# Kernel tuning notes

Hardware: AMD Instinct MI355X
Metric: run time of the kernel (lower is better)

The kernel has to match this reference:

```python
import jax, jax.numpy as jnp
import numpy as np

NUM_BLOCKS_TOTAL = 24  # num_layers(3) * num_blocks(8)
DIL_CYCLE = 8          # dilation = 2 ** (i % 8)


def setup_inputs() -> dict:
    key = jax.random.key(0)
    ks = jax.random.split(key, 12)
    B, C, S, Tq = 256, 32, 32, 256  # batch, residual_ch, skip_ch, queue length
    w = lambda k, sh: jax.random.normal(k, sh, jnp.float32) * 0.1
    return {
        "queues": jax.random.normal(ks[0], (NUM_BLOCKS_TOTAL, B, C, Tq), jnp.float32),
        "x": jax.random.normal(ks[1], (B, 1, 1), jnp.float32),
        "num": jax.random.normal(ks[2], (B, 8, 1), jnp.float32),
        "cat": jax.random.randint(ks[3], (B, 1, 1), 0, 1000),
        "emb_table": w(ks[4], (1000, 16)),
        "W_in": w(ks[5], (C, 25)), "b_in": jnp.zeros((C,), jnp.float32),
        "W_conv": w(ks[6], (NUM_BLOCKS_TOTAL, 2 * C, C, 2)),
        "b_conv": jnp.zeros((NUM_BLOCKS_TOTAL, 2 * C), jnp.float32),
        "W_res": w(ks[7], (NUM_BLOCKS_TOTAL, C, C)),
        "b_res": jnp.zeros((NUM_BLOCKS_TOTAL, C), jnp.float32),
        "W_skip": w(ks[8], (NUM_BLOCKS_TOTAL, S, C)),
        "b_skip": jnp.zeros((NUM_BLOCKS_TOTAL, S), jnp.float32),
        "W_o1": w(ks[9], (128, NUM_BLOCKS_TOTAL * S)), "b_o1": jnp.zeros((128,), jnp.float32),
        "W_o2": w(ks[10], (1, 128)), "b_o2": jnp.zeros((1,), jnp.float32),
    }


def reference(queues, x, num, cat, emb_table, W_in, b_in, W_conv, b_conv,
              W_res, b_res, W_skip, b_skip, W_o1, b_o1, W_o2, b_o2):
    # --- input assembly: concat(x, num, embeds(cat)) along channels, 1 timestep ---
    emb = emb_table[cat[:, 0, 0]][:, :, None]            # [B,16,1]
    inp = jnp.concatenate([x, num, emb], axis=1)          # [B,25,1]
    # pointwise input_conv (kernel_size=1)
    cur = jnp.einsum('oc,bct->bot', W_in, inp) + b_in[None, :, None]  # [B,C,1]

    new_queues = []
    skips = []
    for i in range(NUM_BLOCKS_TOTAL):
        d = 2 ** (i % DIL_CYCLE)
        q = jnp.concatenate([queues[i], cur], axis=2)     # grow queue: [B,C,Tq+1]
        new_queues.append(q)
        # fast_forward: kernel-2 dilated causal conv on last and (last - d) taps
        tap0 = q[:, :, -1 - d]                            # [B,C]
        tap1 = q[:, :, -1]                                # [B,C]
        z = tap0 @ W_conv[i, :, :, 0].T + tap1 @ W_conv[i, :, :, 1].T + b_conv[i]  # [B,2C]
        fz, gz = jnp.split(z, 2, axis=1)
        gated = jnp.tanh(fz) * jax.nn.sigmoid(gz)          # [B,C]
        skips.append(gated @ W_skip[i].T + b_skip[i])      # [B,S]
        cur = (gated @ W_res[i].T + b_res[i] + tap1)[:, :, None]  # residual -> next queue

    sk = jax.nn.relu(jnp.concatenate(skips, axis=1))       # [B, 24*S]
    sk = jax.nn.relu(sk @ W_o1.T + b_o1)                   # [B,128]
    out = (sk @ W_o2.T + b_o2)[:, :, None]                 # [B,1,1]
    return out, jnp.stack(new_queues, axis=0)
```

## Files before the change

### kernel.cpp

```cpp
#include <hip/hip_runtime.h>

#define NBLK 24
#define BATCH 256
#define CCH 32
#define TQ 256
#define TQO 257
#define NCOMP 32
#define BPG 8
#define NCOPY 3072
#define ROWS (NBLK*BATCH*CCH)

typedef float f4a4  __attribute__((ext_vector_type(4), aligned(4)));
typedef float f4a16 __attribute__((ext_vector_type(4)));

__global__ __launch_bounds__(256) void w2w_kernel(
    const float* __restrict__ qin,
    const float* __restrict__ x,
    const float* __restrict__ num,
    const int*   __restrict__ cat,
    const float* __restrict__ emb,
    const float* __restrict__ W_in,  const float* __restrict__ b_in,
    const float* __restrict__ W_conv,const float* __restrict__ b_conv,
    const float* __restrict__ W_res, const float* __restrict__ b_res,
    const float* __restrict__ W_skip,const float* __restrict__ b_skip,
    const float* __restrict__ W_o1,  const float* __restrict__ b_o1,
    const float* __restrict__ W_o2,  const float* __restrict__ b_o2,
    float* __restrict__ out, float* __restrict__ qout)
{
    __shared__ __align__(16) float smem[11264];
    const int tid = threadIdx.x;

    if (blockIdx.x >= NCOMP) {
        const int wid  = (blockIdx.x - NCOMP) * 4 + (tid >> 6);
        const int lane = tid & 63;
        size_t r = (size_t)wid * 16;
        for (int rr = 0; rr < 16; ++rr, ++r) {
            const size_t sb = r * TQ, db = r * TQO;
            const int a = (4 - ((int)r & 3)) & 3;
            if (lane < 63) {
                f4a4 v = *(const f4a4*)(qin + sb + a + 4 * lane);
                *(f4a16*)(qout + db + a + 4 * lane) = v;
            } else {
                #pragma unroll
                for (int e = 0; e < 4; ++e) {
                    const int f = (e < a) ? e : e + 252;
                    qout[db + f] = qin[sb + f];
                }
            }
        }
        return;
    }

    float* s_wc = smem;
    float* s_wr = smem + 4096;
    float* s_ws = smem + 5120;
    float* s_wo = smem + 6144;
    float* s_tc = smem + 10240;
    float* s_g  = smem + 10752;
    float* s_sk = smem + 11008;

    const int bl = tid >> 5;
    const int j  = tid & 31;
    const int sw = j & 7;
    const int b  = blockIdx.x * BPG + bl;

    float cur;
    {
        float acc = b_in[j];
        acc = fmaf(W_in[j * 25 + 0], x[b], acc);
        #pragma unroll
        for (int k = 0; k < 8; ++k) acc = fmaf(W_in[j * 25 + 1 + k], num[b * 8 + k], acc);
        const int ci = cat[b];
        #pragma unroll
        for (int k = 0; k < 16; ++k) acc = fmaf(W_in[j * 25 + 9 + k], emb[ci * 16 + k], acc);
        cur = acc;
    }

    float h0 = 0.f, h1 = 0.f, h2 = 0.f, h3 = 0.f;
    f4a16 rg[10];

    auto issue = [&](int i) {
        const float* pc = W_conv + (size_t)i * 4096;
        #pragma unroll
        for (int k = 0; k < 4; ++k) rg[k] = *(const f4a16*)(pc + (size_t)(tid + 256 * k) * 4);
        rg[4] = *(const f4a16*)(W_res  + (size_t)i * 1024 + tid * 4);
        rg[5] = *(const f4a16*)(W_skip + (size_t)i * 1024 + tid * 4);
        #pragma unroll
        for (int k = 0; k < 4; ++k) {
            const int fi = tid + 256 * k;
            const int m = fi >> 3, p = fi & 7;
            rg[6 + k] = *(const f4a16*)(W_o1 + (size_t)m * 768 + (size_t)i * 32 + p * 4);
        }
    };
    auto commit = [&]() {
        #pragma unroll
        for (int k = 0; k < 4; ++k) *(f4a16*)(s_wc + (tid + 256 * k) * 4) = rg[k];
        *(f4a16*)(s_wr + tid * 4) = rg[4];
        *(f4a16*)(s_ws + tid * 4) = rg[5];
        #pragma unroll
        for (int k = 0; k < 4; ++k) *(f4a16*)(s_wo + (tid + 256 * k) * 4) = rg[6 + k];
    };

    issue(0);
    {
        const float t0 = qin[((size_t)b * CCH + j) * TQ + (TQ - 1)];
        s_tc[bl * 64 + 2 * j]     = t0;
        s_tc[bl * 64 + 2 * j + 1] = cur;
    }
    commit();
    __syncthreads();

    for (int i = 0; i < NBLK; ++i) {
        if (i + 1 < NBLK) issue(i + 1);
        float tap_nxt = 0.f;
        if (i + 1 < NBLK) {
            const int d = 1 << ((i + 1) & 7);
            tap_nxt = qin[((size_t)((i + 1) * BATCH + b) * CCH + j) * TQ + (TQ - d)];
        }
        const float bc0 = b_conv[i * 64 + j];
        const float bc1 = b_conv[i * 64 + 32 + j];
        const float brj = b_res[i * 32 + j];
        const float bsj = b_skip[i * 32 + j];

        const f4a16* wr0 = (const f4a16*)(s_wc) + j * 16;
        const f4a16* wr1 = (const f4a16*)(s_wc) + (32 + j) * 16;
        const f4a16* tcv = (const f4a16*)(s_tc) + bl * 16;
        float z0a = 0.f, z0b = 0.f, z1a = 0.f, z1b = 0.f;
        #pragma unroll
        for (int t = 0; t < 16; ++t) {
            const int k = (t & 8) | ((t ^ sw) & 7);
            const f4a16 w0 = wr0[k], w1 = wr1[k], dv = tcv[k];
            z0a = fmaf(w0.x, dv.x, z0a); z0b = fmaf(w0.y, dv.y, z0b);
            z0a = fmaf(w0.z, dv.z, z0a); z0b = fmaf(w0.w, dv.w, z0b);
            z1a = fmaf(w1.x, dv.x, z1a); z1b = fmaf(w1.y, dv.y, z1b);
            z1a = fmaf(w1.z, dv.z, z1a); z1b = fmaf(w1.w, dv.w, z1b);
        }
        const float z0 = z0a + z0b + bc0;
        const float z1 = z1a + z1b + bc1;
        const float g  = tanhf(z0) * (1.f / (1.f + __expf(-z1)));

        qout[((size_t)(i * BATCH + b) * CCH + j) * TQO + TQ] = cur;

        s_g[bl * 32 + j] = g;
        __builtin_amdgcn_wave_barrier();

        const f4a16* gv  = (const f4a16*)(s_g)  + bl * 8;
        const f4a16* wsv = (const f4a16*)(s_ws) + j * 8;
        const f4a16* wrv = (const f4a16*)(s_wr) + j * 8;
        float ska = bsj, skb = 0.f, cna = brj + cur, cnb = 0.f;
        #pragma unroll
        for (int t = 0; t < 8; ++t) {
            const int k = (t ^ sw) & 7;
            const f4a16 gk = gv[k], wv = wsv[k], rv = wrv[k];
            ska = fmaf(gk.x, wv.x, ska); skb = fmaf(gk.y, wv.y, skb);
            ska = fmaf(gk.z, wv.z, ska); skb = fmaf(gk.w, wv.w, skb);
            cna = fmaf(gk.x, rv.x, cna); cnb = fmaf(gk.y, rv.y, cnb);
            cna = fmaf(gk.z, rv.z, cna); cnb = fmaf(gk.w, rv.w, cnb);
        }
        const float skr = fmaxf(ska + skb, 0.f);
        cur = cna + cnb;

        s_sk[bl * 32 + j] = skr;
        if (i + 1 < NBLK) {
            s_tc[bl * 64 + 2 * j]     = tap_nxt;
            s_tc[bl * 64 + 2 * j + 1] = cur;
        }
        __builtin_amdgcn_wave_barrier();

        const f4a16* skv = (const f4a16*)(s_sk) + bl * 8;
        const f4a16* o0 = (const f4a16*)(s_wo) + j * 8;
        const f4a16* o1 = (const f4a16*)(s_wo) + (32 + j) * 8;
        const f4a16* o2 = (const f4a16*)(s_wo) + (64 + j) * 8;
        const f4a16* o3 = (const f4a16*)(s_wo) + (96 + j) * 8;
        #pragma unroll
        for (int t = 0; t < 8; ++t) {
            const int k = (t ^ sw) & 7;
            const f4a16 rv = skv[k];
            const f4a16 a0 = o0[k], a1 = o1[k], a2 = o2[k], a3 = o3[k];
            h0 = fmaf(rv.x, a0.x, h0); h0 = fmaf(rv.y, a0.y, h0);
            h0 = fmaf(rv.z, a0.z, h0); h0 = fmaf(rv.w, a0.w, h0);
            h1 = fmaf(rv.x, a1.x, h1); h1 = fmaf(rv.y, a1.y, h1);
            h1 = fmaf(rv.z, a1.z, h1); h1 = fmaf(rv.w, a1.w, h1);
            h2 = fmaf(rv.x, a2.x, h2); h2 = fmaf(rv.y, a2.y, h2);
            h2 = fmaf(rv.z, a2.z, h2); h2 = fmaf(rv.w, a2.w, h2);
            h3 = fmaf(rv.x, a3.x, h3); h3 = fmaf(rv.y, a3.y, h3);
            h3 = fmaf(rv.z, a3.z, h3); h3 = fmaf(rv.w, a3.w, h3);
        }

        __syncthreads();
        if (i + 1 < NBLK) commit();
        __syncthreads();
    }

    float p = 0.f;
    p = fmaf(fmaxf(h0 + b_o1[j],      0.f), W_o2[j],      p);
    p = fmaf(fmaxf(h1 + b_o1[j + 32], 0.f), W_o2[j + 32], p);
    p = fmaf(fmaxf(h2 + b_o1[j + 64], 0.f), W_o2[j + 64], p);
    p = fmaf(fmaxf(h3 + b_o1[j + 96], 0.f), W_o2[j + 96], p);
    #pragma unroll
    for (int m = 16; m >= 1; m >>= 1) p += __shfl_xor(p, m);
    if (j == 0) out[b] = p + b_o2[0];
}

extern "C" void kernel_launch(void* const* d_in, const int* in_sizes, int n_in,
                              void* d_out, int out_size, void* d_ws, size_t ws_size,
                              hipStream_t stream) {
    const float* qin    = (const float*)d_in[0];
    const float* x      = (const float*)d_in[1];
    const float* num    = (const float*)d_in[2];
    const int*   cat    = (const int*)  d_in[3];
    const float* emb    = (const float*)d_in[4];
    const float* W_in   = (const float*)d_in[5];
    const float* b_in   = (const float*)d_in[6];
    const float* W_conv = (const float*)d_in[7];
    const float* b_conv = (const float*)d_in[8];
    const float* W_res  = (const float*)d_in[9];
    const float* b_res  = (const float*)d_in[10];
    const float* W_skip = (const float*)d_in[11];
    const float* b_skip = (const float*)d_in[12];
    const float* W_o1   = (const float*)d_in[13];
    const float* b_o1   = (const float*)d_in[14];
    const float* W_o2   = (const float*)d_in[15];
    const float* b_o2   = (const float*)d_in[16];

    float* out  = (float*)d_out;
    float* qout = (float*)d_out + BATCH;

    dim3 grid(NCOMP + NCOPY), block(256);
    hipLaunchKernelGGL(w2w_kernel, grid, block, 0, stream,
                       qin, x, num, cat, emb, W_in, b_in, W_conv, b_conv,
                       W_res, b_res, W_skip, b_skip, W_o1, b_o1, W_o2, b_o2,
                       out, qout);
}
```

Baseline: 504.2 us.

## Spread batch over more compute blocks with two batch rows per block

```diff
diff --git a/kernel.cpp b/kernel.cpp
--- a/kernel.cpp
+++ b/kernel.cpp
@@ -5,8 +5,8 @@
 #define CCH 32
 #define TQ 256
 #define TQO 257
-#define NCOMP 32
-#define BPG 8
+#define NCOMP 128
+#define BPG 2
 #define NCOPY 3072
 #define ROWS (NBLK*BATCH*CCH)
 
@@ -59,13 +59,14 @@
     float* s_g  = smem + 10752;
     float* s_sk = smem + 11008;
 
-    const int bl = tid >> 5;
-    const int j  = tid & 31;
-    const int sw = j & 7;
-    const int b  = blockIdx.x * BPG + bl;
-
-    float cur;
-    {
+    const bool comp = (tid < 64);
+    const int sub = tid >> 5;
+    const int j   = tid & 31;
+    const int sw  = j & 7;
+    const int b   = blockIdx.x * BPG + sub;
+
+    float cur = 0.f;
+    if (comp) {
         float acc = b_in[j];
         acc = fmaf(W_in[j * 25 + 0], x[b], acc);
         #pragma unroll
@@ -102,89 +103,92 @@
     };
 
     issue(0);
-    {
+    if (comp) {
         const float t0 = qin[((size_t)b * CCH + j) * TQ + (TQ - 1)];
-        s_tc[bl * 64 + 2 * j]     = t0;
-        s_tc[bl * 64 + 2 * j + 1] = cur;
+        s_tc[sub * 64 + 2 * j]     = t0;
+        s_tc[sub * 64 + 2 * j + 1] = cur;
     }
     commit();
     __syncthreads();
 
     for (int i = 0; i < NBLK; ++i) {
         if (i + 1 < NBLK) issue(i + 1);
-        float tap_nxt = 0.f;
-        if (i + 1 < NBLK) {
-            const int d = 1 << ((i + 1) & 7);
-            tap_nxt = qin[((size_t)((i + 1) * BATCH + b) * CCH + j) * TQ + (TQ - d)];
-        }
-        const float bc0 = b_conv[i * 64 + j];
-        const float bc1 = b_conv[i * 64 + 32 + j];
-        const float brj = b_res[i * 32 + j];
-        const float bsj = b_skip[i * 32 + j];
-
-        const f4a16* wr0 = (const f4a16*)(s_wc) + j * 16;
-        const f4a16* wr1 = (const f4a16*)(s_wc) + (32 + j) * 16;
-        const f4a16* tcv = (const f4a16*)(s_tc) + bl * 16;
-        float z0a = 0.f, z0b = 0.f, z1a = 0.f, z1b = 0.f;
-        #pragma unroll
-        for (int t = 0; t < 16; ++t) {
-            const int k = (t & 8) | ((t ^ sw) & 7);
-            const f4a16 w0 = wr0[k], w1 = wr1[k], dv = tcv[k];
-            z0a = fmaf(w0.x, dv.x, z0a); z0b = fmaf(w0.y, dv.y, z0b);
-            z0a = fmaf(w0.z, dv.z, z0a); z0b = fmaf(w0.w, dv.w, z0b);
-            z1a = fmaf(w1.x, dv.x, z1a); z1b = fmaf(w1.y, dv.y, z1b);
-            z1a = fmaf(w1.z, dv.z, z1a); z1b = fmaf(w1.w, dv.w, z1b);
-        }
-        const float z0 = z0a + z0b + bc0;
-        const float z1 = z1a + z1b + bc1;
-        const float g  = tanhf(z0) * (1.f / (1.f + __expf(-z1)));
-
-        qout[((size_t)(i * BATCH + b) * CCH + j) * TQO + TQ] = cur;
-
-        s_g[bl * 32 + j] = g;
-        __builtin_amdgcn_wave_barrier();
-
-        const f4a16* gv  = (const f4a16*)(s_g)  + bl * 8;
-        const f4a16* wsv = (const f4a16*)(s_ws) + j * 8;
-        const f4a16* wrv = (const f4a16*)(s_wr) + j * 8;
-        float ska = bsj, skb = 0.f, cna = brj + cur, cnb = 0.f;
-        #pragma unroll
-        for (int t = 0; t < 8; ++t) {
-            const int k = (t ^ sw) & 7;
-            const f4a16 gk = gv[k], wv = wsv[k], rv = wrv[k];
-            ska = fmaf(gk.x, wv.x, ska); skb = fmaf(gk.y, wv.y, skb);
-            ska = fmaf(gk.z, wv.z, ska); skb = fmaf(gk.w, wv.w, skb);
-            cna = fmaf(gk.x, rv.x, cna); cnb = fmaf(gk.y, rv.y, cnb);
-            cna = fmaf(gk.z, rv.z, cna); cnb = fmaf(gk.w, rv.w, cnb);
-        }
-        const float skr = fmaxf(ska + skb, 0.f);
-        cur = cna + cnb;
-
-        s_sk[bl * 32 + j] = skr;
-        if (i + 1 < NBLK) {
-            s_tc[bl * 64 + 2 * j]     = tap_nxt;
-            s_tc[bl * 64 + 2 * j + 1] = cur;
-        }
-        __builtin_amdgcn_wave_barrier();
-
-        const f4a16* skv = (const f4a16*)(s_sk) + bl * 8;
-        const f4a16* o0 = (const f4a16*)(s_wo) + j * 8;
-        const f4a16* o1 = (const f4a16*)(s_wo) + (32 + j) * 8;
-        const f4a16* o2 = (const f4a16*)(s_wo) + (64 + j) * 8;
-        const f4a16* o3 = (const f4a16*)(s_wo) + (96 + j) * 8;
-        #pragma unroll
-        for (int t = 0; t < 8; ++t) {
-            const int k = (t ^ sw) & 7;
-            const f4a16 rv = skv[k];
-            const f4a16 a0 = o0[k], a1 = o1[k], a2 = o2[k], a3 = o3[k];
-            h0 = fmaf(rv.x, a0.x, h0); h0 = fmaf(rv.y, a0.y, h0);
-            h0 = fmaf(rv.z, a0.z, h0); h0 = fmaf(rv.w, a0.w, h0);
-            h1 = fmaf(rv.x, a1.x, h1); h1 = fmaf(rv.y, a1.y, h1);
-            h1 = fmaf(rv.z, a1.z, h1); h1 = fmaf(rv.w, a1.w, h1);
-            h2 = fmaf(rv.x, a2.x, h2); h2 = fmaf(rv.y, a2.y, h2);
-            h2 = fmaf(rv.z, a2.z, h2); h2 = fmaf(rv.w, a2.w, h2);
-            h3 = fmaf(rv.x, a3.x, h3); h3 = fmaf(rv.y, a3.y, h3);
-            h3 = fmaf(rv.z, a3.z, h3); h3 = fmaf(rv.w, a3.w, h3);
+
+        if (comp) {
+            float tap_nxt = 0.f;
+            if (i + 1 < NBLK) {
+                const int d = 1 << ((i + 1) & 7);
+                tap_nxt = qin[((size_t)((i + 1) * BATCH + b) * CCH + j) * TQ + (TQ - d)];
+            }
+            const float bc0 = b_conv[i * 64 + j];
+            const float bc1 = b_conv[i * 64 + 32 + j];
+            const float brj = b_res[i * 32 + j];
+            const float bsj = b_skip[i * 32 + j];
+
+            const f4a16* wr0 = (const f4a16*)(s_wc) + j * 16;
+            const f4a16* wr1 = (const f4a16*)(s_wc) + (32 + j) * 16;
+            const f4a16* tcv = (const f4a16*)(s_tc) + sub * 16;
+            float z0a = 0.f, z0b = 0.f, z1a = 0.f, z1b = 0.f;
+            #pragma unroll
+            for (int t = 0; t < 16; ++t) {
+                const int k = (t & 8) | ((t ^ sw) & 7);
+                const f4a16 w0 = wr0[k], w1 = wr1[k], dv = tcv[k];
+                z0a = fmaf(w0.x, dv.x, z0a); z0b = fmaf(w0.y, dv.y, z0b);
+                z0a = fmaf(w0.z, dv.z, z0a); z0b = fmaf(w0.w, dv.w, z0b);
+                z1a = fmaf(w1.x, dv.x, z1a); z1b = fmaf(w1.y, dv.y, z1b);
+                z1a = fmaf(w1.z, dv.z, z1a); z1b = fmaf(w1.w, dv.w, z1b);
+            }
+            const float z0 = z0a + z0b + bc0;
+            const float z1 = z1a + z1b + bc1;
+            const float g  = tanhf(z0) * (1.f / (1.f + __expf(-z1)));
+
+            qout[((size_t)(i * BATCH + b) * CCH + j) * TQO + TQ] = cur;
+
+            s_g[sub * 32 + j] = g;
+            __builtin_amdgcn_wave_barrier();
+
+            const f4a16* gv  = (const f4a16*)(s_g)  + sub * 8;
+            const f4a16* wsv = (const f4a16*)(s_ws) + j * 8;
+            const f4a16* wrv = (const f4a16*)(s_wr) + j * 8;
+            float ska = bsj, skb = 0.f, cna = brj + cur, cnb = 0.f;
+            #pragma unroll
+            for (int t = 0; t < 8; ++t) {
+                const int k = (t ^ sw) & 7;
+                const f4a16 gk = gv[k], wv = wsv[k], rv = wrv[k];
+                ska = fmaf(gk.x, wv.x, ska); skb = fmaf(gk.y, wv.y, skb);
+                ska = fmaf(gk.z, wv.z, ska); skb = fmaf(gk.w, wv.w, skb);
+                cna = fmaf(gk.x, rv.x, cna); cnb = fmaf(gk.y, rv.y, cnb);
+                cna = fmaf(gk.z, rv.z, cna); cnb = fmaf(gk.w, rv.w, cnb);
+            }
+            const float skr = fmaxf(ska + skb, 0.f);
+            cur = cna + cnb;
+
+            s_sk[sub * 32 + j] = skr;
+            if (i + 1 < NBLK) {
+                s_tc[sub * 64 + 2 * j]     = tap_nxt;
+                s_tc[sub * 64 + 2 * j + 1] = cur;
+            }
+            __builtin_amdgcn_wave_barrier();
+
+            const f4a16* skv = (const f4a16*)(s_sk) + sub * 8;
+            const f4a16* o0 = (const f4a16*)(s_wo) + j * 8;
+            const f4a16* o1 = (const f4a16*)(s_wo) + (32 + j) * 8;
+            const f4a16* o2 = (const f4a16*)(s_wo) + (64 + j) * 8;
+            const f4a16* o3 = (const f4a16*)(s_wo) + (96 + j) * 8;
+            #pragma unroll
+            for (int t = 0; t < 8; ++t) {
+                const int k = (t ^ sw) & 7;
+                const f4a16 rv = skv[k];
+                const f4a16 a0 = o0[k], a1 = o1[k], a2 = o2[k], a3 = o3[k];
+                h0 = fmaf(rv.x, a0.x, h0); h0 = fmaf(rv.y, a0.y, h0);
+                h0 = fmaf(rv.z, a0.z, h0); h0 = fmaf(rv.w, a0.w, h0);
+                h1 = fmaf(rv.x, a1.x, h1); h1 = fmaf(rv.y, a1.y, h1);
+                h1 = fmaf(rv.z, a1.z, h1); h1 = fmaf(rv.w, a1.w, h1);
+                h2 = fmaf(rv.x, a2.x, h2); h2 = fmaf(rv.y, a2.y, h2);
+                h2 = fmaf(rv.z, a2.z, h2); h2 = fmaf(rv.w, a2.w, h2);
+                h3 = fmaf(rv.x, a3.x, h3); h3 = fmaf(rv.y, a3.y, h3);
+                h3 = fmaf(rv.z, a3.z, h3); h3 = fmaf(rv.w, a3.w, h3);
+            }
         }
 
         __syncthreads();
@@ -192,14 +196,16 @@
         __syncthreads();
     }
 
-    float p = 0.f;
-    p = fmaf(fmaxf(h0 + b_o1[j],      0.f), W_o2[j],      p);
-    p = fmaf(fmaxf(h1 + b_o1[j + 32], 0.f), W_o2[j + 32], p);
-    p = fmaf(fmaxf(h2 + b_o1[j + 64], 0.f), W_o2[j + 64], p);
-    p = fmaf(fmaxf(h3 + b_o1[j + 96], 0.f), W_o2[j + 96], p);
-    #pragma unroll
-    for (int m = 16; m >= 1; m >>= 1) p += __shfl_xor(p, m);
-    if (j == 0) out[b] = p + b_o2[0];
+    if (comp) {
+        float p = 0.f;
+        p = fmaf(fmaxf(h0 + b_o1[j],      0.f), W_o2[j],      p);
+        p = fmaf(fmaxf(h1 + b_o1[j + 32], 0.f), W_o2[j + 32], p);
+        p = fmaf(fmaxf(h2 + b_o1[j + 64], 0.f), W_o2[j + 64], p);
+        p = fmaf(fmaxf(h3 + b_o1[j + 96], 0.f), W_o2[j + 96], p);
+        #pragma unroll
+        for (int m = 16; m >= 1; m >>= 1) p += __shfl_xor(p, m);
+        if (j == 0) out[b] = p + b_o2[0];
+    }
 }
 
 extern "C" void kernel_launch(void* const* d_in, const int* in_sizes, int n_in,
```

After: 519.8 us. 1.03x slower.
